# Kernel tuning notes

Measured on AMD Instinct MI355X. Metric: run time of the kernel, lower is better.

Reference implementation:

```python
import jax, jax.numpy as jnp
import numpy as np

B, H, L, N_HEADS = 8192, 1024, 1024, 5

def setup_inputs() -> dict:
    key = jax.random.key(0)
    k1, k2, k3, k4, k5 = jax.random.split(key, 5)
    hidden_state = jax.random.normal(k1, (B, H), dtype=jnp.float32)
    W = jax.random.normal(k2, (N_HEADS, L, H), dtype=jnp.float32) * 0.02  # stacked head weights
    b = jax.random.normal(k3, (N_HEADS, L), dtype=jnp.float32) * 0.02     # stacked head biases
    group = jax.random.randint(k4, (B,), 0, 6, dtype=jnp.int32)
    labels = jax.random.randint(k5, (B,), 0, L, dtype=jnp.int32)
    return {"hidden_state": hidden_state, "W": W, "b": b, "group": group, "labels": labels}

def reference(hidden_state, W, b, group, labels):
    # 5 linear heads in one batched GEMM: [5, B, L]
    all_logits = jnp.einsum("bh,klh->kbl", hidden_state, W) + b[:, None, :]
    # per-row selection by group index (return_logit=True path)
    idx = jnp.clip(group, 0, N_HEADS - 1)
    sel = all_logits[idx, jnp.arange(B)]  # [B, L]
    # group == 5: row filled with broadcast label value (as in original)
    logits = jnp.where((group == 5)[:, None], labels[:, None].astype(jnp.float32), sel)
    return logits
```

## Files before the change

### kernel.cpp

```cpp
#include <hip/hip_runtime.h>
#include <stdint.h>

#define B_ROWS 8192
#define H_DIM 1024
#define L_DIM 1024
#define NH 5

typedef short bf16x8 __attribute__((ext_vector_type(8)));
typedef float f32x4 __attribute__((ext_vector_type(4)));

typedef const __attribute__((address_space(1))) unsigned int* gas_uint_ptr;
typedef __attribute__((address_space(3))) unsigned int* las_uint_ptr;

__device__ __forceinline__ unsigned short f2bf(float f) {
  union { float f; unsigned int u; } v; v.f = f;
  return (unsigned short)((v.u + 0x7FFFu + ((v.u >> 16) & 1u)) >> 16);
}

__device__ __forceinline__ void load_lds16(const void* gsrc, void* ldst) {
  __builtin_amdgcn_global_load_lds((gas_uint_ptr)(uintptr_t)gsrc,
                                   (las_uint_ptr)(uintptr_t)ldst, 16, 0, 0);
}

__global__ void k_bucket(const int* __restrict__ group, int* __restrict__ cnt,
                         int* __restrict__ rowlist) {
  __shared__ int lcnt[NH];
  __shared__ int lbase[NH];
  int t = threadIdx.x;
  if (t < NH) lcnt[t] = 0;
  __syncthreads();
  int b = blockIdx.x * 256 + t;
  int g = group[b];
  int lpos = -1;
  if (g < NH) lpos = atomicAdd(&lcnt[g], 1);
  __syncthreads();
  if (t < NH) lbase[t] = atomicAdd(&cnt[t], lcnt[t]);
  __syncthreads();
  if (g < NH) rowlist[g * B_ROWS + lbase[g] + lpos] = b;
}

__global__ void k_fill(const int* __restrict__ group, const int* __restrict__ labels,
                       float* __restrict__ out) {
  int b = blockIdx.x;
  if (group[b] != NH) return;
  float v = (float)labels[b];
  float4 vv = make_float4(v, v, v, v);
  float4* o = (float4*)(out + (size_t)b * L_DIM);
  o[threadIdx.x] = vv;
}

__global__ void k_convw(const float* __restrict__ W, unsigned short* __restrict__ Wb) {
  int i = blockIdx.x * 256 + threadIdx.x;
  float4 w = ((const float4*)W)[i];
  ushort4 o;
  o.x = f2bf(w.x); o.y = f2bf(w.y); o.z = f2bf(w.z); o.w = f2bf(w.w);
  ((ushort4*)Wb)[i] = o;
}

__global__ void k_gather(const float* __restrict__ hidden, const int* __restrict__ cnt,
                         const int* __restrict__ rowlist, unsigned short* __restrict__ Hg) {
  int g = blockIdx.x >> 13;
  int i = blockIdx.x & (B_ROWS - 1);
  if (i >= cnt[g]) return;
  int base = 0;
#pragma unroll
  for (int k = 0; k < NH; k++) base += (k < g) ? cnt[k] : 0;
  int b = rowlist[g * B_ROWS + i];
  float4 h = ((const float4*)(hidden + (size_t)b * H_DIM))[threadIdx.x];
  ushort4 o;
  o.x = f2bf(h.x); o.y = f2bf(h.y); o.z = f2bf(h.z); o.w = f2bf(h.w);
  ((ushort4*)(Hg + (size_t)(base + i) * H_DIM))[threadIdx.x] = o;
}

__global__ __launch_bounds__(256, 2)
void k_gemm(const unsigned short* __restrict__ Hg, const unsigned short* __restrict__ Wb,
            const float* __restrict__ bias, const int* __restrict__ cnt,
            const int* __restrict__ rowlist, float* __restrict__ out) {
  const int head = blockIdx.z;
  const int cntg = cnt[head];
  const int rowbase = blockIdx.y * 128;
  if (rowbase >= cntg) return;
  int base = 0;
#pragma unroll
  for (int k = 0; k < NH; k++) base += (k < head) ? cnt[k] : 0;
  const int n0 = blockIdx.x * 128;

  __shared__ __align__(16) unsigned short As[128 * 64];
  __shared__ __align__(16) unsigned short Bs[128 * 64];

  const int t = threadIdx.x;
  const int wave = t >> 6, lane = t & 63;
  const int quad = lane >> 4, c16 = lane & 15;
  const int wm = (wave & 1) * 64, wn = (wave >> 1) * 64;

  f32x4 acc[4][4] = {};

  const unsigned short* Wg = Wb + (size_t)head * L_DIM * H_DIM;

  for (int kt = 0; kt < H_DIM; kt += 64) {
    __syncthreads();
#pragma unroll
    for (int p = 0; p < 4; p++) {
      int c = p * 256 + t;
      int row = c >> 3;
      int ks = ((c & 7) ^ (row & 7)) * 8;
      int gar = base + rowbase + row;
      gar = gar < (B_ROWS - 1) ? gar : (B_ROWS - 1);
      load_lds16(Hg + (size_t)gar * H_DIM + kt + ks, As + c * 8);
      load_lds16(Wg + (size_t)(n0 + row) * H_DIM + kt + ks, Bs + c * 8);
    }
    __syncthreads();
#pragma unroll
    for (int kk = 0; kk < 64; kk += 32) {
      bf16x8 af[4], bf[4];
      const int sw = c16 & 7;
      const int colb = (kk >> 4) << 1;
#pragma unroll
      for (int i = 0; i < 4; i++) {
        int row = wm + i * 16 + c16;
        int cl = (colb + quad) ^ sw;
        af[i] = *(const bf16x8*)(As + row * 64 + cl * 8);
      }
#pragma unroll
      for (int j = 0; j < 4; j++) {
        int row = wn + j * 16 + c16;
        int cl = (colb + quad) ^ sw;
        bf[j] = *(const bf16x8*)(Bs + row * 64 + cl * 8);
      }
#pragma unroll
      for (int i = 0; i < 4; i++)
#pragma unroll
        for (int j = 0; j < 4; j++)
          acc[i][j] = __builtin_amdgcn_mfma_f32_16x16x32_bf16(af[i], bf[j], acc[i][j], 0, 0, 0);
    }
  }

  const int* rl = rowlist + head * B_ROWS + rowbase;
#pragma unroll
  for (int i = 0; i < 4; i++) {
    int rloc0 = wm + i * 16 + quad * 4;
#pragma unroll
    for (int r = 0; r < 4; r++) {
      int idx = rloc0 + r;
      if (rowbase + idx < cntg) {
        int orow = rl[idx];
        float* orowp = out + (size_t)orow * L_DIM + n0;
#pragma unroll
        for (int j = 0; j < 4; j++) {
          int n = wn + j * 16 + c16;
          orowp[n] = acc[i][j][r] + bias[head * L_DIM + n0 + n];
        }
      }
    }
  }
}

extern "C" void kernel_launch(void* const* d_in, const int* in_sizes, int n_in,
                              void* d_out, int out_size, void* d_ws, size_t ws_size,
                              hipStream_t stream) {
  const float* hidden = (const float*)d_in[0];
  const float* W      = (const float*)d_in[1];
  const float* bias   = (const float*)d_in[2];
  const int* group    = (const int*)d_in[3];
  const int* labels   = (const int*)d_in[4];
  float* out = (float*)d_out;

  char* ws = (char*)d_ws;
  int* cnt = (int*)ws;
  int* rowlist = (int*)(ws + 256);
  unsigned short* Wb = (unsigned short*)(ws + (1 << 18));
  unsigned short* Hg = (unsigned short*)(ws + (1 << 18) + (size_t)NH * L_DIM * H_DIM * 2);

  hipMemsetAsync(cnt, 0, 64, stream);
  k_bucket<<<B_ROWS / 256, 256, 0, stream>>>(group, cnt, rowlist);
  k_fill<<<B_ROWS, 256, 0, stream>>>(group, labels, out);
  k_convw<<<NH * L_DIM * H_DIM / 1024, 256, 0, stream>>>(W, Wb);
  k_gather<<<NH * B_ROWS, 256, 0, stream>>>(hidden, cnt, rowlist, Hg);
  k_gemm<<<dim3(L_DIM / 128, B_ROWS / 128, NH), 256, 0, stream>>>(Hg, Wb, bias, cnt, rowlist, out);
}
```

Baseline: 148.6 us.

## Fuse prep kernels, gather rows via rowlist in GEMM, double-buffer LDS tiles

The bucket, fill, W-convert and gather kernels are merged into one prep kernel. It converts hidden rows to bf16 in place and builds per-head row lists using a global atomic per row. The GEMM now reads A rows indirectly through the row list instead of a compacted gathered buffer. It also double-buffers the LDS tiles so the next K tile loads while MFMAs run on the current one. This removes three launches and the separate gather pass. In exchange, rowlist order becomes nondeterministic, LDS use doubles, and A loads become scattered rows.

```diff
diff --git a/kernel.cpp b/kernel.cpp
--- a/kernel.cpp
+++ b/kernel.cpp
@@ -22,94 +22,93 @@
                                    (las_uint_ptr)(uintptr_t)ldst, 16, 0, 0);
 }
 
-__global__ void k_bucket(const int* __restrict__ group, int* __restrict__ cnt,
-                         int* __restrict__ rowlist) {
-  __shared__ int lcnt[NH];
-  __shared__ int lbase[NH];
-  int t = threadIdx.x;
-  if (t < NH) lcnt[t] = 0;
-  __syncthreads();
-  int b = blockIdx.x * 256 + t;
-  int g = group[b];
-  int lpos = -1;
-  if (g < NH) lpos = atomicAdd(&lcnt[g], 1);
-  __syncthreads();
-  if (t < NH) lbase[t] = atomicAdd(&cnt[t], lcnt[t]);
-  __syncthreads();
-  if (g < NH) rowlist[g * B_ROWS + lbase[g] + lpos] = b;
-}
-
-__global__ void k_fill(const int* __restrict__ group, const int* __restrict__ labels,
+__global__ void k_prep(const float* __restrict__ hidden, const float* __restrict__ W,
+                       const int* __restrict__ group, const int* __restrict__ labels,
+                       int* __restrict__ cnt, int* __restrict__ rowlist,
+                       unsigned short* __restrict__ Hb, unsigned short* __restrict__ Wb,
                        float* __restrict__ out) {
-  int b = blockIdx.x;
-  if (group[b] != NH) return;
-  float v = (float)labels[b];
-  float4 vv = make_float4(v, v, v, v);
-  float4* o = (float4*)(out + (size_t)b * L_DIM);
-  o[threadIdx.x] = vv;
-}
-
-__global__ void k_convw(const float* __restrict__ W, unsigned short* __restrict__ Wb) {
-  int i = blockIdx.x * 256 + threadIdx.x;
-  float4 w = ((const float4*)W)[i];
-  ushort4 o;
-  o.x = f2bf(w.x); o.y = f2bf(w.y); o.z = f2bf(w.z); o.w = f2bf(w.w);
-  ((ushort4*)Wb)[i] = o;
-}
-
-__global__ void k_gather(const float* __restrict__ hidden, const int* __restrict__ cnt,
-                         const int* __restrict__ rowlist, unsigned short* __restrict__ Hg) {
-  int g = blockIdx.x >> 13;
-  int i = blockIdx.x & (B_ROWS - 1);
-  if (i >= cnt[g]) return;
-  int base = 0;
-#pragma unroll
-  for (int k = 0; k < NH; k++) base += (k < g) ? cnt[k] : 0;
-  int b = rowlist[g * B_ROWS + i];
-  float4 h = ((const float4*)(hidden + (size_t)b * H_DIM))[threadIdx.x];
-  ushort4 o;
-  o.x = f2bf(h.x); o.y = f2bf(h.y); o.z = f2bf(h.z); o.w = f2bf(h.w);
-  ((ushort4*)(Hg + (size_t)(base + i) * H_DIM))[threadIdx.x] = o;
+  const int blk = blockIdx.x;
+  const int t = threadIdx.x;
+  if (blk < B_ROWS) {
+    int g = group[blk];
+    if (g == NH) {
+      float v = (float)labels[blk];
+      ((float4*)(out + (size_t)blk * L_DIM))[t] = make_float4(v, v, v, v);
+    } else {
+      float4 h = ((const float4*)(hidden + (size_t)blk * H_DIM))[t];
+      ushort4 o;
+      o.x = f2bf(h.x); o.y = f2bf(h.y); o.z = f2bf(h.z); o.w = f2bf(h.w);
+      ((ushort4*)(Hb + (size_t)blk * H_DIM))[t] = o;
+      if (t == 0) {
+        int pos = atomicAdd(&cnt[g], 1);
+        rowlist[g * B_ROWS + pos] = blk;
+      }
+    }
+  } else {
+    int i = (blk - B_ROWS) * 256 + t;
+    float4 w = ((const float4*)W)[i];
+    ushort4 o;
+    o.x = f2bf(w.x); o.y = f2bf(w.y); o.z = f2bf(w.z); o.w = f2bf(w.w);
+    ((ushort4*)Wb)[i] = o;
+  }
 }
 
 __global__ __launch_bounds__(256, 2)
-void k_gemm(const unsigned short* __restrict__ Hg, const unsigned short* __restrict__ Wb,
+void k_gemm(const unsigned short* __restrict__ Hb, const unsigned short* __restrict__ Wb,
             const float* __restrict__ bias, const int* __restrict__ cnt,
             const int* __restrict__ rowlist, float* __restrict__ out) {
   const int head = blockIdx.z;
   const int cntg = cnt[head];
   const int rowbase = blockIdx.y * 128;
   if (rowbase >= cntg) return;
-  int base = 0;
-#pragma unroll
-  for (int k = 0; k < NH; k++) base += (k < head) ? cnt[k] : 0;
   const int n0 = blockIdx.x * 128;
 
-  __shared__ __align__(16) unsigned short As[128 * 64];
-  __shared__ __align__(16) unsigned short Bs[128 * 64];
+  __shared__ __align__(16) unsigned short As[2][128 * 64];
+  __shared__ __align__(16) unsigned short Bs[2][128 * 64];
 
   const int t = threadIdx.x;
   const int wave = t >> 6, lane = t & 63;
   const int quad = lane >> 4, c16 = lane & 15;
   const int wm = (wave & 1) * 64, wn = (wave >> 1) * 64;
 
+  const unsigned short* Wg = Wb + (size_t)head * L_DIM * H_DIM;
+  const int* rl = rowlist + head * B_ROWS;
+
+  const unsigned short* srcA[4];
+  const unsigned short* srcB[4];
+  int ldso[4];
+#pragma unroll
+  for (int p = 0; p < 4; p++) {
+    int c = p * 256 + t;
+    int row = c >> 3;
+    int ks = ((c & 7) ^ (row & 7)) * 8;
+    int idx = rowbase + row;
+    idx = idx < cntg ? idx : cntg - 1;
+    int rA = rl[idx];
+    srcA[p] = Hb + (size_t)rA * H_DIM + ks;
+    srcB[p] = Wg + (size_t)(n0 + row) * H_DIM + ks;
+    ldso[p] = c * 8;
+  }
+
   f32x4 acc[4][4] = {};
 
-  const unsigned short* Wg = Wb + (size_t)head * L_DIM * H_DIM;
+#pragma unroll
+  for (int p = 0; p < 4; p++) {
+    load_lds16(srcA[p], &As[0][ldso[p]]);
+    load_lds16(srcB[p], &Bs[0][ldso[p]]);
+  }
+  __syncthreads();
 
   for (int kt = 0; kt < H_DIM; kt += 64) {
-    __syncthreads();
+    const int cur = (kt >> 6) & 1;
+    if (kt + 64 < H_DIM) {
+      const int nxt = cur ^ 1;
 #pragma unroll
-    for (int p = 0; p < 4; p++) {
-      int c = p * 256 + t;
-      int row = c >> 3;
-      int ks = ((c & 7) ^ (row & 7)) * 8;
-      int gar = base + rowbase + row;
-      gar = gar < (B_ROWS - 1) ? gar : (B_ROWS - 1);
-      load_lds16(Hg + (size_t)gar * H_DIM + kt + ks, As + c * 8);
-      load_lds16(Wg + (size_t)(n0 + row) * H_DIM + kt + ks, Bs + c * 8);
+      for (int p = 0; p < 4; p++) {
+        load_lds16(srcA[p] + kt + 64, &As[nxt][ldso[p]]);
+        load_lds16(srcB[p] + kt + 64, &Bs[nxt][ldso[p]]);
+      }
     }
-    __syncthreads();
 #pragma unroll
     for (int kk = 0; kk < 64; kk += 32) {
       bf16x8 af[4], bf[4];
@@ -119,13 +118,13 @@
       for (int i = 0; i < 4; i++) {
         int row = wm + i * 16 + c16;
         int cl = (colb + quad) ^ sw;
-        af[i] = *(const bf16x8*)(As + row * 64 + cl * 8);
+        af[i] = *(const bf16x8*)(&As[cur][row * 64 + cl * 8]);
       }
 #pragma unroll
       for (int j = 0; j < 4; j++) {
         int row = wn + j * 16 + c16;
         int cl = (colb + quad) ^ sw;
-        bf[j] = *(const bf16x8*)(Bs + row * 64 + cl * 8);
+        bf[j] = *(const bf16x8*)(&Bs[cur][row * 64 + cl * 8]);
       }
 #pragma unroll
       for (int i = 0; i < 4; i++)
@@ -133,9 +132,9 @@
         for (int j = 0; j < 4; j++)
           acc[i][j] = __builtin_amdgcn_mfma_f32_16x16x32_bf16(af[i], bf[j], acc[i][j], 0, 0, 0);
     }
+    __syncthreads();
   }
 
-  const int* rl = rowlist + head * B_ROWS + rowbase;
 #pragma unroll
   for (int i = 0; i < 4; i++) {
     int rloc0 = wm + i * 16 + quad * 4;
@@ -143,7 +142,7 @@
     for (int r = 0; r < 4; r++) {
       int idx = rloc0 + r;
       if (rowbase + idx < cntg) {
-        int orow = rl[idx];
+        int orow = rl[rowbase + idx];
         float* orowp = out + (size_t)orow * L_DIM + n0;
 #pragma unroll
         for (int j = 0; j < 4; j++) {
@@ -169,12 +168,10 @@
   int* cnt = (int*)ws;
   int* rowlist = (int*)(ws + 256);
   unsigned short* Wb = (unsigned short*)(ws + (1 << 18));
-  unsigned short* Hg = (unsigned short*)(ws + (1 << 18) + (size_t)NH * L_DIM * H_DIM * 2);
+  unsigned short* Hb = (unsigned short*)(ws + (1 << 18) + (size_t)NH * L_DIM * H_DIM * 2);
 
   hipMemsetAsync(cnt, 0, 64, stream);
-  k_bucket<<<B_ROWS / 256, 256, 0, stream>>>(group, cnt, rowlist);
-  k_fill<<<B_ROWS, 256, 0, stream>>>(group, labels, out);
-  k_convw<<<NH * L_DIM * H_DIM / 1024, 256, 0, stream>>>(W, Wb);
-  k_gather<<<NH * B_ROWS, 256, 0, stream>>>(hidden, cnt, rowlist, Hg);
-  k_gemm<<<dim3(L_DIM / 128, B_ROWS / 128, NH), 256, 0, stream>>>(Hg, Wb, bias, cnt, rowlist, out);
+  k_prep<<<B_ROWS + NH * L_DIM * H_DIM / 1024, 256, 0, stream>>>(
+      hidden, W, group, labels, cnt, rowlist, Hb, Wb, out);
+  k_gemm<<<dim3(L_DIM / 128, B_ROWS / 128, NH), 256, 0, stream>>>(Hb, Wb, bias, cnt, rowlist, out);
 }
```

Result: slower. 197.3 us (+32.8%).
